# Kernel optimization log

Measured on AMD Instinct MI355X. Metric: run time of the kernel, lower is better.

The kernel has to match this reference:

```python
import jax, jax.numpy as jnp
import numpy as np

NUM_HEADS = 8
NUM_POINTS = 4


def _bilinear_sample(value_hw, locs, H, W):
    """grid_sample(mode='bilinear', align_corners=False, padding_mode='zeros').
    value_hw: [B, heads, H*W, hd]; locs: [B, Nq, heads, P, 2] in [0,1].
    Returns [B, Nq, heads, P, hd]."""
    B, Nq, heads, P, _ = locs.shape
    hd = value_hw.shape[-1]
    # torch maps g in [-1,1] -> pixel ((g+1)*size-1)/2; with g = 2*loc-1 this is loc*size - 0.5
    x = locs[..., 0] * W - 0.5
    y = locs[..., 1] * H - 0.5
    x0 = jnp.floor(x); y0 = jnp.floor(y)
    wx = x - x0; wy = y - y0
    ix0 = x0.astype(jnp.int32); iy0 = y0.astype(jnp.int32)
    ix1 = ix0 + 1; iy1 = iy0 + 1

    def gather(iy, ix):
        valid = (ix >= 0) & (ix < W) & (iy >= 0) & (iy < H)
        flat = jnp.clip(iy, 0, H - 1) * W + jnp.clip(ix, 0, W - 1)  # [B,Nq,heads,P]
        flat_t = flat.transpose(0, 2, 1, 3).reshape(B, heads, Nq * P)
        v = jnp.take_along_axis(value_hw, flat_t[..., None], axis=2)  # [B,heads,Nq*P,hd]
        v = v.reshape(B, heads, Nq, P, hd).transpose(0, 2, 1, 3, 4)
        return v * valid[..., None].astype(v.dtype)

    out = (gather(iy0, ix0) * ((1 - wx) * (1 - wy))[..., None]
           + gather(iy0, ix1) * (wx * (1 - wy))[..., None]
           + gather(iy1, ix0) * ((1 - wx) * wy)[..., None]
           + gather(iy1, ix1) * (wx * wy)[..., None])
    return out


def setup_inputs() -> dict:
    key = jax.random.key(0)
    ks = jax.random.split(key, 12)
    B, Nq, C, H, W = 4, 8192, 256, 128, 128
    heads, P = NUM_HEADS, NUM_POINTS
    s = 1.0 / np.sqrt(C)
    return {
        "query": jax.random.normal(ks[0], (B, Nq, C), jnp.float32),
        "reference_points": jax.random.uniform(ks[1], (B, Nq, 2), jnp.float32),
        "value": jax.random.normal(ks[2], (B, H * W, C), jnp.float32),
        "W_off": jax.random.normal(ks[3], (C, heads * P * 2), jnp.float32) * s,
        "b_off": jax.random.normal(ks[4], (heads * P * 2,), jnp.float32) * 0.5,
        "W_attn": jax.random.normal(ks[5], (C, heads * P), jnp.float32) * s,
        "b_attn": jax.random.normal(ks[6], (heads * P,), jnp.float32) * 0.1,
        "W_v": jax.random.normal(ks[7], (C, C), jnp.float32) * s,
        "b_v": jax.random.normal(ks[8], (C,), jnp.float32) * 0.1,
        "W_out": jax.random.normal(ks[9], (C, C), jnp.float32) * s,
        "b_out": jax.random.normal(ks[10], (C,), jnp.float32) * 0.1,
        "H": H,
        "W": W,
    }


def reference(query, reference_points, value, W_off, b_off, W_attn, b_attn,
              W_v, b_v, W_out, b_out, H, W):
    B, Nq, C = query.shape
    heads, P = NUM_HEADS, NUM_POINTS
    hd = C // heads

    offsets = (query @ W_off + b_off).reshape(B, Nq, heads, P, 2)
    attn = jax.nn.softmax((query @ W_attn + b_attn).reshape(B, Nq, heads, P), axis=-1)

    off_x = offsets[..., 0] / float(W) * 0.1
    off_y = offsets[..., 1] / float(H) * 0.1
    locs = reference_points[:, :, None, None, :] + jnp.stack([off_x, off_y], axis=-1)
    locs = jnp.clip(locs, 0.0, 1.0)  # [B,Nq,heads,P,2]

    # value projection -> [B, heads, H*W, hd]
    v = (value @ W_v + b_v).reshape(B, H * W, heads, hd).transpose(0, 2, 1, 3)

    sampled = _bilinear_sample(v, locs, H, W)            # [B,Nq,heads,P,hd]
    agg = jnp.einsum('bnhp,bnhpd->bnhd', attn, sampled)  # weighted sum over points
    out = agg.reshape(B, Nq, C) @ W_out + b_out
    return out
```

## Files before the change

kernel.cpp:

```cpp
#include <hip/hip_runtime.h>
#include <cstdint>

#define NB 4
#define NQ 8192
#define NC 256
#define IH 128
#define IW 128
#define NHW (IH * IW)
#define NHEADS 8
#define NP 4
#define NHD 32

typedef __bf16 bf16x8 __attribute__((ext_vector_type(8)));
typedef float f32x4 __attribute__((ext_vector_type(4)));

union FragCast { uint4 q; bf16x8 v; };

__device__ __forceinline__ unsigned int f2bf(float f) {
    unsigned int u = __float_as_uint(f);
    return (u + 0x7FFFu + ((u >> 16) & 1u)) >> 16;
}
__device__ __forceinline__ float bf2f(unsigned short s) {
    return __uint_as_float(((unsigned int)s) << 16);
}

__global__ __launch_bounds__(256) void k_pack(
    const float* __restrict__ Wv, const float* __restrict__ Wout,
    const float* __restrict__ Woff, const float* __restrict__ Wattn,
    unsigned short* __restrict__ pkv, unsigned short* __restrict__ pko,
    unsigned short* __restrict__ pkq)
{
    const int tid = blockIdx.x * 256 + threadIdx.x;
    if (tid < 4096) {
        const float* src = (tid & 2048) ? Wout : Wv;
        unsigned short* dst = (tid & 2048) ? pko : pkv;
        const int rem = tid & 2047;
        const int kt = rem >> 8, col = rem & 255;
        unsigned short* d = dst + (size_t)(kt * 256 + col) * 32;
        const float* s = src + (size_t)kt * 32 * 256 + col;
#pragma unroll
        for (int j = 0; j < 32; ++j)
            d[j] = (unsigned short)f2bf(s[(size_t)j * 256]);
    } else {
        const int rem = tid - 4096;
        const int kt = rem / 96, col = rem % 96;
        unsigned short* d = pkq + (size_t)(kt * 96 + col) * 32;
        const float* s; int stride;
        if (col < 64) { s = Woff + col; stride = 64; }
        else          { s = Wattn + (col - 64); stride = 32; }
        s += (size_t)kt * 32 * stride;
#pragma unroll
        for (int j = 0; j < 32; ++j)
            d[j] = (unsigned short)f2bf(s[(size_t)j * stride]);
    }
}

#define VP_TPB 4
__global__ __launch_bounds__(512) void k_vproj(
    const float* __restrict__ value, const unsigned short* __restrict__ Bpk,
    const float* __restrict__ bv, unsigned short* __restrict__ vproj)
{
    const int t = threadIdx.x;
    const int l = t & 63, w = t >> 6;
    const int mh = w & 1, cg = w >> 1;

    __shared__ unsigned short A[2][64 * 256];

    uint4 bq[8][4];
#pragma unroll
    for (int kt = 0; kt < 8; ++kt)
#pragma unroll
        for (int i = 0; i < 4; ++i)
            bq[kt][i] = *reinterpret_cast<const uint4*>(
                Bpk + (size_t)kt * 8192 + (size_t)(cg * 4 + i) * 512 +
                (l & 15) * 32 + (l >> 4) * 8);

    float bb[4];
#pragma unroll
    for (int i = 0; i < 4; ++i) bb[i] = bv[cg * 64 + i * 16 + (l & 15)];

    const size_t tile0 = (size_t)blockIdx.x * VP_TPB;

    float4 st[8];
#pragma unroll
    for (int i = 0; i < 8; ++i) {
        const int chunk = i * 512 + t;
        const int row = chunk >> 6, k0 = (chunk & 63) * 4;
        st[i] = *reinterpret_cast<const float4*>(&value[(tile0 * 64 + row) * NC + k0]);
    }
#pragma unroll
    for (int i = 0; i < 8; ++i) {
        const int chunk = i * 512 + t;
        const int row = chunk >> 6, k0 = (chunk & 63) * 4;
        unsigned int byte = (unsigned int)(row * 512 + k0 * 2) ^ (unsigned int)((row & 7) << 4);
        *reinterpret_cast<uint2*>(reinterpret_cast<char*>(A[0]) + byte) =
            make_uint2(f2bf(st[i].x) | (f2bf(st[i].y) << 16),
                       f2bf(st[i].z) | (f2bf(st[i].w) << 16));
    }
    __syncthreads();

    for (int tt = 0; tt < VP_TPB; ++tt) {
        const int cur = tt & 1;
        if (tt + 1 < VP_TPB) {
#pragma unroll
            for (int i = 0; i < 8; ++i) {
                const int chunk = i * 512 + t;
                const int row = chunk >> 6, k0 = (chunk & 63) * 4;
                st[i] = *reinterpret_cast<const float4*>(
                    &value[((tile0 + tt + 1) * 64 + row) * NC + k0]);
            }
        }

        f32x4 acc[2][4];
#pragma unroll
        for (int m = 0; m < 2; ++m)
#pragma unroll
            for (int i = 0; i < 4; ++i) acc[m][i] = (f32x4)(bb[i]);

#pragma unroll
        for (int kt = 0; kt < 8; ++kt) {
#pragma unroll
            for (int m = 0; m < 2; ++m) {
                const int arow = mh * 32 + m * 16 + (l & 15);
                unsigned int abyte = (unsigned int)(arow * 512 + (kt * 32 + (l >> 4) * 8) * 2)
                                   ^ (unsigned int)((arow & 7) << 4);
                FragCast af;
                af.q = *reinterpret_cast<const uint4*>(reinterpret_cast<const char*>(A[cur]) + abyte);
#pragma unroll
                for (int i = 0; i < 4; ++i) {
                    FragCast bfc; bfc.q = bq[kt][i];
                    acc[m][i] = __builtin_amdgcn_mfma_f32_16x16x32_bf16(af.v, bfc.v, acc[m][i], 0, 0, 0);
                }
            }
        }

        const size_t rowbase = (tile0 + tt) * 64;
#pragma unroll
        for (int m = 0; m < 2; ++m)
#pragma unroll
            for (int i = 0; i < 4; ++i) {
                const int col = cg * 64 + i * 16 + (l & 15);
#pragma unroll
                for (int j = 0; j < 4; ++j) {
                    const size_t row = rowbase + mh * 32 + m * 16 + (l >> 4) * 4 + j;
                    vproj[row * NC + col] = (unsigned short)f2bf(acc[m][i][j]);
                }
            }

        if (tt + 1 < VP_TPB) {
#pragma unroll
            for (int i = 0; i < 8; ++i) {
                const int chunk = i * 512 + t;
                const int row = chunk >> 6, k0 = (chunk & 63) * 4;
                unsigned int byte = (unsigned int)(row * 512 + k0 * 2) ^ (unsigned int)((row & 7) << 4);
                *reinterpret_cast<uint2*>(reinterpret_cast<char*>(A[cur ^ 1]) + byte) =
                    make_uint2(f2bf(st[i].x) | (f2bf(st[i].y) << 16),
                               f2bf(st[i].z) | (f2bf(st[i].w) << 16));
            }
            __syncthreads();
        }
    }
}

__global__ __launch_bounds__(256) void k_offattn(
    const float* __restrict__ query, const float* __restrict__ refp,
    const unsigned short* __restrict__ Bpk, const float* __restrict__ boff,
    const float* __restrict__ battn,
    float* __restrict__ locs, float* __restrict__ attnw)
{
    const int t = threadIdx.x;
    const int l = t & 63, w = t >> 6;
    const size_t q0 = (size_t)blockIdx.x * 32;

    __shared__ unsigned short A[32 * 256];
    __shared__ float refs[32][2];

#pragma unroll
    for (int i = 0; i < 8; ++i) {
        const int chunk = i * 256 + t;
        const int row = chunk >> 6;
        const int k0 = (chunk & 63) * 4;
        const float4 v4 = *reinterpret_cast<const float4*>(&query[(q0 + row) * NC + k0]);
        const unsigned int lo = f2bf(v4.x) | (f2bf(v4.y) << 16);
        const unsigned int hi = f2bf(v4.z) | (f2bf(v4.w) << 16);
        unsigned int byte = (unsigned int)(row * 512 + k0 * 2);
        byte ^= (unsigned int)((row & 7) << 4);
        *reinterpret_cast<uint2*>(reinterpret_cast<char*>(A) + byte) = make_uint2(lo, hi);
    }
    if (t < 64) reinterpret_cast<float*>(refs)[t] = refp[q0 * 2 + t];
    __syncthreads();

    const int rt = w >> 1, ctbase = (w & 1) * 3;
    const int arow = rt * 16 + (l & 15);
    const int achunk = l >> 4;

    f32x4 acc[3];
#pragma unroll
    for (int i = 0; i < 3; ++i) acc[i] = (f32x4)(0.f);

#pragma unroll
    for (int kt = 0; kt < 8; ++kt) {
        unsigned int abyte = (unsigned int)(arow * 512 + (kt * 32 + achunk * 8) * 2);
        abyte ^= (unsigned int)((arow & 7) << 4);
        FragCast af;
        af.q = *reinterpret_cast<const uint4*>(reinterpret_cast<const char*>(A) + abyte);
        const unsigned short* bbase = Bpk + (size_t)kt * (96 * 32) + (l & 15) * 32 + achunk * 8;
#pragma unroll
        for (int i = 0; i < 3; ++i) {
            const int ct = ctbase + i;
            FragCast bfc;
            bfc.q = *reinterpret_cast<const uint4*>(bbase + ct * 512);
            acc[i] = __builtin_amdgcn_mfma_f32_16x16x32_bf16(af.v, bfc.v, acc[i], 0, 0, 0);
        }
    }

#pragma unroll
    for (int i = 0; i < 3; ++i) {
        const int col = (ctbase + i) * 16 + (l & 15);
        if (col < 64) {
            const float bias = boff[col];
            const int xy = col & 1;
#pragma unroll
            for (int j = 0; j < 4; ++j) {
                const int row = rt * 16 + (l >> 4) * 4 + j;
                float off = acc[i][j] + bias;
                float loc = refs[row][xy] + off * (0.1f / 128.0f);
                loc = fminf(fmaxf(loc, 0.f), 1.f);
                locs[(q0 + row) * 64 + col] = loc;
            }
        } else {
            const int lc = col - 64;
            const float bias = battn[lc];
#pragma unroll
            for (int j = 0; j < 4; ++j) {
                const int row = rt * 16 + (l >> 4) * 4 + j;
                float v = acc[i][j] + bias;
                float m = fmaxf(v, __shfl_xor(v, 1));
                m = fmaxf(m, __shfl_xor(m, 2));
                float e = __expf(v - m);
                float s = e + __shfl_xor(e, 1);
                s = s + __shfl_xor(s, 2);
                attnw[(q0 + row) * 32 + lc] = e / s;
            }
        }
    }
}

__global__ __launch_bounds__(256) void k_sample(
    const unsigned short* __restrict__ vproj, const float* __restrict__ locs,
    const float* __restrict__ attnw, const unsigned short* __restrict__ Bpk,
    const float* __restrict__ bout, float* __restrict__ out)
{
    const int t = threadIdx.x;
    const int l = t & 63, w = t >> 6;
    const size_t q0 = (size_t)blockIdx.x * 16;
    const int b = (int)(q0 / NQ);

    __shared__ float locs_s[16][64];
    __shared__ float attn_s[16][32];
    __shared__ unsigned short agg[16 * 256];

    {
        const float4* ls = reinterpret_cast<const float4*>(locs + q0 * 64);
        float4* ld = reinterpret_cast<float4*>(&locs_s[0][0]);
        ld[t] = ls[t];
        const float2* as = reinterpret_cast<const float2*>(attnw + q0 * 32);
        float2* ad = reinterpret_cast<float2*>(&attn_s[0][0]);
        ad[t] = as[t];
    }
    __syncthreads();

    const int rhalf = l >> 5, h = (l >> 2) & 7, c = l & 3;
    const unsigned short* __restrict__ vb =
        vproj + (size_t)b * NHW * NC + h * NHD + c * 8;

#pragma unroll
    for (int it = 0; it < 2; ++it) {
        const int r = w * 4 + it * 2 + rhalf;
        float wts[16];
        uint4 vals[16];
#pragma unroll
        for (int p = 0; p < 4; ++p) {
            const float lx = locs_s[r][h * 8 + p * 2 + 0];
            const float ly = locs_s[r][h * 8 + p * 2 + 1];
            const float aw = attn_s[r][h * 4 + p];
            const float x = lx * (float)IW - 0.5f;
            const float y = ly * (float)IH - 0.5f;
            const float x0f = floorf(x), y0f = floorf(y);
            const float wx = x - x0f, wy = y - y0f;
            const int ix0 = (int)x0f, iy0 = (int)y0f;
            const int ix1 = ix0 + 1, iy1 = iy0 + 1;
            const int cx0 = max(ix0, 0), cy0 = max(iy0, 0);
            const int cx1 = min(ix1, IW - 1), cy1 = min(iy1, IH - 1);
            const float vx0 = (ix0 >= 0) ? 1.f : 0.f;
            const float vy0 = (iy0 >= 0) ? 1.f : 0.f;
            const float vx1 = (ix1 < IW) ? 1.f : 0.f;
            const float vy1 = (iy1 < IH) ? 1.f : 0.f;
            wts[p * 4 + 0] = aw * ((1.f - wx) * (1.f - wy) * vx0 * vy0);
            wts[p * 4 + 1] = aw * (wx * (1.f - wy) * vx1 * vy0);
            wts[p * 4 + 2] = aw * ((1.f - wx) * wy * vx0 * vy1);
            wts[p * 4 + 3] = aw * (wx * wy * vx1 * vy1);
            vals[p * 4 + 0] = *reinterpret_cast<const uint4*>(vb + (size_t)(cy0 * IW + cx0) * NC);
            vals[p * 4 + 1] = *reinterpret_cast<const uint4*>(vb + (size_t)(cy0 * IW + cx1) * NC);
            vals[p * 4 + 2] = *reinterpret_cast<const uint4*>(vb + (size_t)(cy1 * IW + cx0) * NC);
            vals[p * 4 + 3] = *reinterpret_cast<const uint4*>(vb + (size_t)(cy1 * IW + cx1) * NC);
        }
        float acc[8];
#pragma unroll
        for (int e = 0; e < 8; ++e) acc[e] = 0.f;
#pragma unroll
        for (int j = 0; j < 16; ++j) {
            const unsigned short* u = reinterpret_cast<const unsigned short*>(&vals[j]);
            const float wj = wts[j];
#pragma unroll
            for (int e = 0; e < 8; ++e) acc[e] = fmaf(wj, bf2f(u[e]), acc[e]);
        }
        uint4 pk;
        pk.x = f2bf(acc[0]) | (f2bf(acc[1]) << 16);
        pk.y = f2bf(acc[2]) | (f2bf(acc[3]) << 16);
        pk.z = f2bf(acc[4]) | (f2bf(acc[5]) << 16);
        pk.w = f2bf(acc[6]) | (f2bf(acc[7]) << 16);
        unsigned int byte = (unsigned int)(r * 512 + (h * NHD + c * 8) * 2);
        byte ^= (unsigned int)((r & 7) << 4);
        *reinterpret_cast<uint4*>(reinterpret_cast<char*>(agg) + byte) = pk;
    }
    __syncthreads();

    const int arow = l & 15;
    const int achunk = l >> 4;
    f32x4 acc2[4];
#pragma unroll
    for (int i = 0; i < 4; ++i) acc2[i] = (f32x4)(0.f);

#pragma unroll
    for (int kt = 0; kt < 8; ++kt) {
        unsigned int abyte = (unsigned int)(arow * 512 + (kt * 32 + achunk * 8) * 2);
        abyte ^= (unsigned int)((arow & 7) << 4);
        FragCast af;
        af.q = *reinterpret_cast<const uint4*>(reinterpret_cast<const char*>(agg) + abyte);
        const unsigned short* bbase = Bpk + (size_t)kt * 8192 + (l & 15) * 32 + achunk * 8;
#pragma unroll
        for (int i = 0; i < 4; ++i) {
            const int ct = w * 4 + i;
            FragCast bfc;
            bfc.q = *reinterpret_cast<const uint4*>(bbase + ct * 512);
            acc2[i] = __builtin_amdgcn_mfma_f32_16x16x32_bf16(af.v, bfc.v, acc2[i], 0, 0, 0);
        }
    }

#pragma unroll
    for (int i = 0; i < 4; ++i) {
        const int col = (w * 4 + i) * 16 + (l & 15);
        const float bbv = bout[col];
#pragma unroll
        for (int j = 0; j < 4; ++j) {
            const size_t row = q0 + (l >> 4) * 4 + j;
            out[row * NC + col] = acc2[i][j] + bbv;
        }
    }
}

extern "C" void kernel_launch(void* const* d_in, const int* in_sizes, int n_in,
                              void* d_out, int out_size, void* d_ws, size_t ws_size,
                              hipStream_t stream) {
    const float* query = (const float*)d_in[0];
    const float* refp  = (const float*)d_in[1];
    const float* value = (const float*)d_in[2];
    const float* Woff  = (const float*)d_in[3];
    const float* boff  = (const float*)d_in[4];
    const float* Wattn = (const float*)d_in[5];
    const float* battn = (const float*)d_in[6];
    const float* Wv    = (const float*)d_in[7];
    const float* bv    = (const float*)d_in[8];
    const float* Wout  = (const float*)d_in[9];
    const float* bout  = (const float*)d_in[10];
    float* out = (float*)d_out;

    unsigned short* vproj = (unsigned short*)d_ws;
    float* locs  = (float*)(vproj + (size_t)NB * NHW * NC);
    float* attnw = locs + (size_t)NB * NQ * NHEADS * NP * 2;
    unsigned short* WvPk   = (unsigned short*)(attnw + (size_t)NB * NQ * NHEADS * NP);
    unsigned short* WoutPk = WvPk + (size_t)NC * NC;
    unsigned short* WqPk   = WoutPk + (size_t)NC * NC;

    k_pack<<<dim3(19), dim3(256), 0, stream>>>(Wv, Wout, Woff, Wattn, WvPk, WoutPk, WqPk);
    k_vproj<<<dim3(256), dim3(512), 0, stream>>>(value, WvPk, bv, vproj);
    k_offattn<<<dim3(NB * NQ / 32), dim3(256), 0, stream>>>(query, refp, WqPk, boff,
                                                            battn, locs, attnw);
    k_sample<<<dim3(NB * NQ / 16), dim3(256), 0, stream>>>(vproj, locs, attnw, WoutPk, bout, out);
}
```

Before: 82.72 us.

## Fuse offset/attention projection into sampling kernel, eliminating locs/attn round-trip

Merges the query offset/attention-weight GEMM with softmax into the sampling+output-projection kernel, so locations and attention weights go straight to shared memory and never through global workspace. This removes one kernel launch and the global write/read of the locs and attnw buffers. The query tile buffer is reused for the aggregated samples, and a scheduling barrier is placed after the gather loads. In exchange, each 16-query block now does the small GEMM with uneven wave work (two of the four waves run a second pass), and the stages within a block are serialized.

```diff
diff --git a/kernel.cpp b/kernel.cpp
--- a/kernel.cpp
+++ b/kernel.cpp
@@ -162,200 +162,174 @@
     }
 }
 
-__global__ __launch_bounds__(256) void k_offattn(
+__global__ __launch_bounds__(256) void k_fused(
     const float* __restrict__ query, const float* __restrict__ refp,
-    const unsigned short* __restrict__ Bpk, const float* __restrict__ boff,
-    const float* __restrict__ battn,
-    float* __restrict__ locs, float* __restrict__ attnw)
-{
-    const int t = threadIdx.x;
-    const int l = t & 63, w = t >> 6;
-    const size_t q0 = (size_t)blockIdx.x * 32;
-
-    __shared__ unsigned short A[32 * 256];
-    __shared__ float refs[32][2];
-
-#pragma unroll
-    for (int i = 0; i < 8; ++i) {
-        const int chunk = i * 256 + t;
-        const int row = chunk >> 6;
-        const int k0 = (chunk & 63) * 4;
-        const float4 v4 = *reinterpret_cast<const float4*>(&query[(q0 + row) * NC + k0]);
-        const unsigned int lo = f2bf(v4.x) | (f2bf(v4.y) << 16);
-        const unsigned int hi = f2bf(v4.z) | (f2bf(v4.w) << 16);
-        unsigned int byte = (unsigned int)(row * 512 + k0 * 2);
-        byte ^= (unsigned int)((row & 7) << 4);
-        *reinterpret_cast<uint2*>(reinterpret_cast<char*>(A) + byte) = make_uint2(lo, hi);
-    }
-    if (t < 64) reinterpret_cast<float*>(refs)[t] = refp[q0 * 2 + t];
-    __syncthreads();
-
-    const int rt = w >> 1, ctbase = (w & 1) * 3;
-    const int arow = rt * 16 + (l & 15);
-    const int achunk = l >> 4;
-
-    f32x4 acc[3];
-#pragma unroll
-    for (int i = 0; i < 3; ++i) acc[i] = (f32x4)(0.f);
-
-#pragma unroll
-    for (int kt = 0; kt < 8; ++kt) {
-        unsigned int abyte = (unsigned int)(arow * 512 + (kt * 32 + achunk * 8) * 2);
-        abyte ^= (unsigned int)((arow & 7) << 4);
-        FragCast af;
-        af.q = *reinterpret_cast<const uint4*>(reinterpret_cast<const char*>(A) + abyte);
-        const unsigned short* bbase = Bpk + (size_t)kt * (96 * 32) + (l & 15) * 32 + achunk * 8;
-#pragma unroll
-        for (int i = 0; i < 3; ++i) {
-            const int ct = ctbase + i;
-            FragCast bfc;
-            bfc.q = *reinterpret_cast<const uint4*>(bbase + ct * 512);
-            acc[i] = __builtin_amdgcn_mfma_f32_16x16x32_bf16(af.v, bfc.v, acc[i], 0, 0, 0);
-        }
-    }
-
-#pragma unroll
-    for (int i = 0; i < 3; ++i) {
-        const int col = (ctbase + i) * 16 + (l & 15);
-        if (col < 64) {
-            const float bias = boff[col];
-            const int xy = col & 1;
-#pragma unroll
-            for (int j = 0; j < 4; ++j) {
-                const int row = rt * 16 + (l >> 4) * 4 + j;
-                float off = acc[i][j] + bias;
-                float loc = refs[row][xy] + off * (0.1f / 128.0f);
-                loc = fminf(fmaxf(loc, 0.f), 1.f);
-                locs[(q0 + row) * 64 + col] = loc;
-            }
-        } else {
-            const int lc = col - 64;
-            const float bias = battn[lc];
-#pragma unroll
-            for (int j = 0; j < 4; ++j) {
-                const int row = rt * 16 + (l >> 4) * 4 + j;
-                float v = acc[i][j] + bias;
-                float m = fmaxf(v, __shfl_xor(v, 1));
-                m = fmaxf(m, __shfl_xor(m, 2));
-                float e = __expf(v - m);
-                float s = e + __shfl_xor(e, 1);
-                s = s + __shfl_xor(s, 2);
-                attnw[(q0 + row) * 32 + lc] = e / s;
-            }
-        }
-    }
-}
-
-__global__ __launch_bounds__(256) void k_sample(
-    const unsigned short* __restrict__ vproj, const float* __restrict__ locs,
-    const float* __restrict__ attnw, const unsigned short* __restrict__ Bpk,
-    const float* __restrict__ bout, float* __restrict__ out)
+    const unsigned short* __restrict__ Bq, const float* __restrict__ boff,
+    const float* __restrict__ battn, const unsigned short* __restrict__ vproj,
+    const unsigned short* __restrict__ Bo, const float* __restrict__ bout,
+    float* __restrict__ out)
 {
     const int t = threadIdx.x;
     const int l = t & 63, w = t >> 6;
     const size_t q0 = (size_t)blockIdx.x * 16;
     const int b = (int)(q0 / NQ);
 
+    __shared__ unsigned short A[16 * 256];
     __shared__ float locs_s[16][64];
     __shared__ float attn_s[16][32];
-    __shared__ unsigned short agg[16 * 256];
+    __shared__ float refs[16][2];
+
+#pragma unroll
+    for (int i = 0; i < 4; ++i) {
+        const int chunk = i * 256 + t;
+        const int row = chunk >> 6, k0 = (chunk & 63) * 4;
+        const float4 v4 = *reinterpret_cast<const float4*>(&query[(q0 + row) * NC + k0]);
+        unsigned int byte = (unsigned int)(row * 512 + k0 * 2) ^ (unsigned int)((row & 7) << 4);
+        *reinterpret_cast<uint2*>(reinterpret_cast<char*>(A) + byte) =
+            make_uint2(f2bf(v4.x) | (f2bf(v4.y) << 16),
+                       f2bf(v4.z) | (f2bf(v4.w) << 16));
+    }
+    if (t < 32) reinterpret_cast<float*>(refs)[t] = refp[q0 * 2 + t];
+    __syncthreads();
 
     {
-        const float4* ls = reinterpret_cast<const float4*>(locs + q0 * 64);
-        float4* ld = reinterpret_cast<float4*>(&locs_s[0][0]);
-        ld[t] = ls[t];
-        const float2* as = reinterpret_cast<const float2*>(attnw + q0 * 32);
-        float2* ad = reinterpret_cast<float2*>(&attn_s[0][0]);
-        ad[t] = as[t];
+        const int arow = l & 15, achunk = l >> 4;
+#pragma unroll
+        for (int pass = 0; pass < 2; ++pass) {
+            if (pass == 1 && w >= 2) break;
+            const int ct = pass == 0 ? w : 4 + w;
+            f32x4 acc = (f32x4)(0.f);
+#pragma unroll
+            for (int kt = 0; kt < 8; ++kt) {
+                unsigned int abyte = (unsigned int)(arow * 512 + (kt * 32 + achunk * 8) * 2)
+                                   ^ (unsigned int)((arow & 7) << 4);
+                FragCast af;
+                af.q = *reinterpret_cast<const uint4*>(reinterpret_cast<const char*>(A) + abyte);
+                FragCast bfc;
+                bfc.q = *reinterpret_cast<const uint4*>(
+                    Bq + (size_t)kt * 3072 + (size_t)(ct * 16 + arow) * 32 + achunk * 8);
+                acc = __builtin_amdgcn_mfma_f32_16x16x32_bf16(af.v, bfc.v, acc, 0, 0, 0);
+            }
+            const int col = ct * 16 + arow;
+            if (col < 64) {
+                const float bias = boff[col];
+                const int xy = col & 1;
+#pragma unroll
+                for (int j = 0; j < 4; ++j) {
+                    const int row = achunk * 4 + j;
+                    float off = acc[j] + bias;
+                    float loc = refs[row][xy] + off * (0.1f / 128.0f);
+                    locs_s[row][col] = fminf(fmaxf(loc, 0.f), 1.f);
+                }
+            } else {
+                const int lc = col - 64;
+                const float bias = battn[lc];
+#pragma unroll
+                for (int j = 0; j < 4; ++j) {
+                    const int row = achunk * 4 + j;
+                    float v = acc[j] + bias;
+                    float m = fmaxf(v, __shfl_xor(v, 1));
+                    m = fmaxf(m, __shfl_xor(m, 2));
+                    float e = __expf(v - m);
+                    float s = e + __shfl_xor(e, 1);
+                    s = s + __shfl_xor(s, 2);
+                    attn_s[row][lc] = e / s;
+                }
+            }
+        }
     }
     __syncthreads();
 
-    const int rhalf = l >> 5, h = (l >> 2) & 7, c = l & 3;
-    const unsigned short* __restrict__ vb =
-        vproj + (size_t)b * NHW * NC + h * NHD + c * 8;
-
-#pragma unroll
-    for (int it = 0; it < 2; ++it) {
-        const int r = w * 4 + it * 2 + rhalf;
-        float wts[16];
-        uint4 vals[16];
-#pragma unroll
-        for (int p = 0; p < 4; ++p) {
-            const float lx = locs_s[r][h * 8 + p * 2 + 0];
-            const float ly = locs_s[r][h * 8 + p * 2 + 1];
-            const float aw = attn_s[r][h * 4 + p];
-            const float x = lx * (float)IW - 0.5f;
-            const float y = ly * (float)IH - 0.5f;
-            const float x0f = floorf(x), y0f = floorf(y);
-            const float wx = x - x0f, wy = y - y0f;
-            const int ix0 = (int)x0f, iy0 = (int)y0f;
-            const int ix1 = ix0 + 1, iy1 = iy0 + 1;
-            const int cx0 = max(ix0, 0), cy0 = max(iy0, 0);
-            const int cx1 = min(ix1, IW - 1), cy1 = min(iy1, IH - 1);
-            const float vx0 = (ix0 >= 0) ? 1.f : 0.f;
-            const float vy0 = (iy0 >= 0) ? 1.f : 0.f;
-            const float vx1 = (ix1 < IW) ? 1.f : 0.f;
-            const float vy1 = (iy1 < IH) ? 1.f : 0.f;
-            wts[p * 4 + 0] = aw * ((1.f - wx) * (1.f - wy) * vx0 * vy0);
-            wts[p * 4 + 1] = aw * (wx * (1.f - wy) * vx1 * vy0);
-            wts[p * 4 + 2] = aw * ((1.f - wx) * wy * vx0 * vy1);
-            wts[p * 4 + 3] = aw * (wx * wy * vx1 * vy1);
-            vals[p * 4 + 0] = *reinterpret_cast<const uint4*>(vb + (size_t)(cy0 * IW + cx0) * NC);
-            vals[p * 4 + 1] = *reinterpret_cast<const uint4*>(vb + (size_t)(cy0 * IW + cx1) * NC);
-            vals[p * 4 + 2] = *reinterpret_cast<const uint4*>(vb + (size_t)(cy1 * IW + cx0) * NC);
-            vals[p * 4 + 3] = *reinterpret_cast<const uint4*>(vb + (size_t)(cy1 * IW + cx1) * NC);
-        }
-        float acc[8];
-#pragma unroll
-        for (int e = 0; e < 8; ++e) acc[e] = 0.f;
-#pragma unroll
-        for (int j = 0; j < 16; ++j) {
-            const unsigned short* u = reinterpret_cast<const unsigned short*>(&vals[j]);
-            const float wj = wts[j];
-#pragma unroll
-            for (int e = 0; e < 8; ++e) acc[e] = fmaf(wj, bf2f(u[e]), acc[e]);
-        }
-        uint4 pk;
-        pk.x = f2bf(acc[0]) | (f2bf(acc[1]) << 16);
-        pk.y = f2bf(acc[2]) | (f2bf(acc[3]) << 16);
-        pk.z = f2bf(acc[4]) | (f2bf(acc[5]) << 16);
-        pk.w = f2bf(acc[6]) | (f2bf(acc[7]) << 16);
-        unsigned int byte = (unsigned int)(r * 512 + (h * NHD + c * 8) * 2);
-        byte ^= (unsigned int)((r & 7) << 4);
-        *reinterpret_cast<uint4*>(reinterpret_cast<char*>(agg) + byte) = pk;
+    {
+        const int rhalf = l >> 5, h = (l >> 2) & 7, c = l & 3;
+        const unsigned short* __restrict__ vb =
+            vproj + (size_t)b * NHW * NC + h * NHD + c * 8;
+
+#pragma unroll
+        for (int it = 0; it < 2; ++it) {
+            const int r = w * 4 + it * 2 + rhalf;
+            float wts[16];
+            uint4 vals[16];
+#pragma unroll
+            for (int p = 0; p < 4; ++p) {
+                const float lx = locs_s[r][h * 8 + p * 2 + 0];
+                const float ly = locs_s[r][h * 8 + p * 2 + 1];
+                const float aw = attn_s[r][h * 4 + p];
+                const float x = lx * (float)IW - 0.5f;
+                const float y = ly * (float)IH - 0.5f;
+                const float x0f = floorf(x), y0f = floorf(y);
+                const float wx = x - x0f, wy = y - y0f;
+                const int ix0 = (int)x0f, iy0 = (int)y0f;
+                const int ix1 = ix0 + 1, iy1 = iy0 + 1;
+                const int cx0 = max(ix0, 0), cy0 = max(iy0, 0);
+                const int cx1 = min(ix1, IW - 1), cy1 = min(iy1, IH - 1);
+                const float vx0 = (ix0 >= 0) ? 1.f : 0.f;
+                const float vy0 = (iy0 >= 0) ? 1.f : 0.f;
+                const float vx1 = (ix1 < IW) ? 1.f : 0.f;
+                const float vy1 = (iy1 < IH) ? 1.f : 0.f;
+                wts[p * 4 + 0] = aw * ((1.f - wx) * (1.f - wy) * vx0 * vy0);
+                wts[p * 4 + 1] = aw * (wx * (1.f - wy) * vx1 * vy0);
+                wts[p * 4 + 2] = aw * ((1.f - wx) * wy * vx0 * vy1);
+                wts[p * 4 + 3] = aw * (wx * wy * vx1 * vy1);
+                vals[p * 4 + 0] = *reinterpret_cast<const uint4*>(vb + (size_t)(cy0 * IW + cx0) * NC);
+                vals[p * 4 + 1] = *reinterpret_cast<const uint4*>(vb + (size_t)(cy0 * IW + cx1) * NC);
+                vals[p * 4 + 2] = *reinterpret_cast<const uint4*>(vb + (size_t)(cy1 * IW + cx0) * NC);
+                vals[p * 4 + 3] = *reinterpret_cast<const uint4*>(vb + (size_t)(cy1 * IW + cx1) * NC);
+            }
+            __builtin_amdgcn_sched_barrier(0);
+            float acc[8];
+#pragma unroll
+            for (int e = 0; e < 8; ++e) acc[e] = 0.f;
+#pragma unroll
+            for (int j = 0; j < 16; ++j) {
+                const unsigned short* u = reinterpret_cast<const unsigned short*>(&vals[j]);
+                const float wj = wts[j];
+#pragma unroll
+                for (int e = 0; e < 8; ++e) acc[e] = fmaf(wj, bf2f(u[e]), acc[e]);
+            }
+            uint4 pk;
+            pk.x = f2bf(acc[0]) | (f2bf(acc[1]) << 16);
+            pk.y = f2bf(acc[2]) | (f2bf(acc[3]) << 16);
+            pk.z = f2bf(acc[4]) | (f2bf(acc[5]) << 16);
+            pk.w = f2bf(acc[6]) | (f2bf(acc[7]) << 16);
+            unsigned int byte = (unsigned int)(r * 512 + (h * NHD + c * 8) * 2)
+                              ^ (unsigned int)((r & 7) << 4);
+            *reinterpret_cast<uint4*>(reinterpret_cast<char*>(A) + byte) = pk;
+        }
     }
     __syncthreads();
 
-    const int arow = l & 15;
-    const int achunk = l >> 4;
-    f32x4 acc2[4];
-#pragma unroll
-    for (int i = 0; i < 4; ++i) acc2[i] = (f32x4)(0.f);
-
-#pragma unroll
-    for (int kt = 0; kt < 8; ++kt) {
-        unsigned int abyte = (unsigned int)(arow * 512 + (kt * 32 + achunk * 8) * 2);
-        abyte ^= (unsigned int)((arow & 7) << 4);
-        FragCast af;
-        af.q = *reinterpret_cast<const uint4*>(reinterpret_cast<const char*>(agg) + abyte);
-        const unsigned short* bbase = Bpk + (size_t)kt * 8192 + (l & 15) * 32 + achunk * 8;
+    {
+        const int arow = l & 15, achunk = l >> 4;
+        f32x4 acc2[4];
+#pragma unroll
+        for (int i = 0; i < 4; ++i) acc2[i] = (f32x4)(0.f);
+
+#pragma unroll
+        for (int kt = 0; kt < 8; ++kt) {
+            unsigned int abyte = (unsigned int)(arow * 512 + (kt * 32 + achunk * 8) * 2)
+                               ^ (unsigned int)((arow & 7) << 4);
+            FragCast af;
+            af.q = *reinterpret_cast<const uint4*>(reinterpret_cast<const char*>(A) + abyte);
+            const unsigned short* bbase = Bo + (size_t)kt * 8192 + arow * 32 + achunk * 8;
+#pragma unroll
+            for (int i = 0; i < 4; ++i) {
+                const int ct = w * 4 + i;
+                FragCast bfc;
+                bfc.q = *reinterpret_cast<const uint4*>(bbase + (size_t)ct * 512);
+                acc2[i] = __builtin_amdgcn_mfma_f32_16x16x32_bf16(af.v, bfc.v, acc2[i], 0, 0, 0);
+            }
+        }
+
 #pragma unroll
         for (int i = 0; i < 4; ++i) {
-            const int ct = w * 4 + i;
-            FragCast bfc;
-            bfc.q = *reinterpret_cast<const uint4*>(bbase + ct * 512);
-            acc2[i] = __builtin_amdgcn_mfma_f32_16x16x32_bf16(af.v, bfc.v, acc2[i], 0, 0, 0);
-        }
-    }
-
-#pragma unroll
-    for (int i = 0; i < 4; ++i) {
-        const int col = (w * 4 + i) * 16 + (l & 15);
-        const float bbv = bout[col];
-#pragma unroll
-        for (int j = 0; j < 4; ++j) {
-            const size_t row = q0 + (l >> 4) * 4 + j;
-            out[row * NC + col] = acc2[i][j] + bbv;
+            const int col = (w * 4 + i) * 16 + arow;
+            const float bbv = bout[col];
+#pragma unroll
+            for (int j = 0; j < 4; ++j) {
+                const size_t row = q0 + achunk * 4 + j;
+                out[row * NC + col] = acc2[i][j] + bbv;
+            }
         }
     }
 }
@@ -376,16 +350,13 @@
     const float* bout  = (const float*)d_in[10];
     float* out = (float*)d_out;
 
-    unsigned short* vproj = (unsigned short*)d_ws;
-    float* locs  = (float*)(vproj + (size_t)NB * NHW * NC);
-    float* attnw = locs + (size_t)NB * NQ * NHEADS * NP * 2;
-    unsigned short* WvPk   = (unsigned short*)(attnw + (size_t)NB * NQ * NHEADS * NP);
+    unsigned short* vproj  = (unsigned short*)d_ws;
+    unsigned short* WvPk   = vproj + (size_t)NB * NHW * NC;
     unsigned short* WoutPk = WvPk + (size_t)NC * NC;
     unsigned short* WqPk   = WoutPk + (size_t)NC * NC;
 
     k_pack<<<dim3(19), dim3(256), 0, stream>>>(Wv, Wout, Woff, Wattn, WvPk, WoutPk, WqPk);
     k_vproj<<<dim3(256), dim3(512), 0, stream>>>(value, WvPk, bv, vproj);
-    k_offattn<<<dim3(NB * NQ / 32), dim3(256), 0, stream>>>(query, refp, WqPk, boff,
-                                                            battn, locs, attnw);
-    k_sample<<<dim3(NB * NQ / 16), dim3(256), 0, stream>>>(vproj, locs, attnw, WoutPk, bout, out);
-}
+    k_fused<<<dim3(NB * NQ / 16), dim3(256), 0, stream>>>(query, refp, WqPk, boff, battn,
+                                                          vproj, WoutPk, bout, out);
+}
```

Measured after the change: 74.13 us. 1.12x faster.

## Store value projection per batch-head plane and split sampling from output projection

Applied to the files above, without the earlier changes.

The value projection is now written as contiguous [B, head, pixel, 32] planes instead of [B, pixel, 256]. The fused sample+outproj kernel is split into a gather kernel, where each block handles one (batch, head) pair for 64 queries, and a separate double-buffered MFMA output-projection kernel that keeps weights in registers. The goal is better cache locality for the gathers, since each head plane is 1 MB, and more efficient GEMM tiling. The cost is an extra round trip for the bf16 aggregate through global memory, one more launch, and scattered 2-byte stores in vproj.

```diff
diff --git a/kernel.cpp b/kernel.cpp
--- a/kernel.cpp
+++ b/kernel.cpp
@@ -140,10 +140,13 @@
 #pragma unroll
             for (int i = 0; i < 4; ++i) {
                 const int col = cg * 64 + i * 16 + (l & 15);
+                const int hh = col >> 5, dd = col & 31;
 #pragma unroll
                 for (int j = 0; j < 4; ++j) {
                     const size_t row = rowbase + mh * 32 + m * 16 + (l >> 4) * 4 + j;
-                    vproj[row * NC + col] = (unsigned short)f2bf(acc[m][i][j]);
+                    const size_t bidx = row >> 14, pix = row & (NHW - 1);
+                    vproj[(((bidx << 3) + hh) * (size_t)NHW + pix) * NHD + dd] =
+                        (unsigned short)f2bf(acc[m][i][j]);
                 }
             }
 
@@ -246,116 +249,193 @@
     }
 }
 
-__global__ __launch_bounds__(256) void k_sample(
+__global__ __launch_bounds__(256) void k_gather(
     const unsigned short* __restrict__ vproj, const float* __restrict__ locs,
-    const float* __restrict__ attnw, const unsigned short* __restrict__ Bpk,
+    const float* __restrict__ attnw, unsigned short* __restrict__ agg)
+{
+    const int bid = blockIdx.x;
+    const int x = bid & 7;
+    const int rem = bid >> 3;
+    const int pg = rem >> 7;
+    const int chunk = rem & 127;
+    const int pair = pg * 8 + x;
+    const int b = pair >> 3, h = pair & 7;
+    const int t = threadIdx.x;
+
+    const size_t qrow0 = (size_t)b * NQ + chunk * 64;
+
+    __shared__ float lc[64][8];
+    __shared__ float at[64][4];
+
+    if (t < 128) {
+        const int q = t >> 1, part = t & 1;
+        *reinterpret_cast<float4*>(&lc[q][part * 4]) =
+            *reinterpret_cast<const float4*>(&locs[(qrow0 + q) * 64 + h * 8 + part * 4]);
+    } else if (t < 192) {
+        const int q = t - 128;
+        *reinterpret_cast<float4*>(&at[q][0]) =
+            *reinterpret_cast<const float4*>(&attnw[(qrow0 + q) * 32 + h * 4]);
+    }
+    __syncthreads();
+
+    const int q = t >> 2, c = t & 3;
+    const char* __restrict__ plane =
+        reinterpret_cast<const char*>(vproj + (size_t)pair * NHW * NHD);
+    const unsigned int laneoff = (unsigned int)(c * 16);
+
+    float wts[16];
+    unsigned int offs[16];
+#pragma unroll
+    for (int p = 0; p < 4; ++p) {
+        const float lx = lc[q][p * 2 + 0];
+        const float ly = lc[q][p * 2 + 1];
+        const float aw = at[q][p];
+        const float xx = lx * (float)IW - 0.5f;
+        const float yy = ly * (float)IH - 0.5f;
+        const float x0f = floorf(xx), y0f = floorf(yy);
+        const float wx = xx - x0f, wy = yy - y0f;
+        const int ix0 = (int)x0f, iy0 = (int)y0f;
+        const int ix1 = ix0 + 1, iy1 = iy0 + 1;
+        const int cx0 = max(ix0, 0), cy0 = max(iy0, 0);
+        const int cx1 = min(ix1, IW - 1), cy1 = min(iy1, IH - 1);
+        const float vx0 = (ix0 >= 0) ? 1.f : 0.f;
+        const float vy0 = (iy0 >= 0) ? 1.f : 0.f;
+        const float vx1 = (ix1 < IW) ? 1.f : 0.f;
+        const float vy1 = (iy1 < IH) ? 1.f : 0.f;
+        wts[p * 4 + 0] = aw * ((1.f - wx) * (1.f - wy) * vx0 * vy0);
+        wts[p * 4 + 1] = aw * (wx * (1.f - wy) * vx1 * vy0);
+        wts[p * 4 + 2] = aw * ((1.f - wx) * wy * vx0 * vy1);
+        wts[p * 4 + 3] = aw * (wx * wy * vx1 * vy1);
+        offs[p * 4 + 0] = (unsigned int)(cy0 * IW + cx0) * 64u + laneoff;
+        offs[p * 4 + 1] = (unsigned int)(cy0 * IW + cx1) * 64u + laneoff;
+        offs[p * 4 + 2] = (unsigned int)(cy1 * IW + cx0) * 64u + laneoff;
+        offs[p * 4 + 3] = (unsigned int)(cy1 * IW + cx1) * 64u + laneoff;
+    }
+
+    uint4 vals[16];
+#pragma unroll
+    for (int j = 0; j < 16; ++j)
+        vals[j] = *reinterpret_cast<const uint4*>(plane + offs[j]);
+
+    float acc[8];
+#pragma unroll
+    for (int e = 0; e < 8; ++e) acc[e] = 0.f;
+#pragma unroll
+    for (int j = 0; j < 16; ++j) {
+        const unsigned short* u = reinterpret_cast<const unsigned short*>(&vals[j]);
+        const float wj = wts[j];
+#pragma unroll
+        for (int e = 0; e < 8; ++e) acc[e] = fmaf(wj, bf2f(u[e]), acc[e]);
+    }
+
+    uint4 pk;
+    pk.x = f2bf(acc[0]) | (f2bf(acc[1]) << 16);
+    pk.y = f2bf(acc[2]) | (f2bf(acc[3]) << 16);
+    pk.z = f2bf(acc[4]) | (f2bf(acc[5]) << 16);
+    pk.w = f2bf(acc[6]) | (f2bf(acc[7]) << 16);
+    *reinterpret_cast<uint4*>(&agg[(qrow0 + q) * NC + h * NHD + c * 8]) = pk;
+}
+
+#define OP_TPB 4
+__global__ __launch_bounds__(512) void k_outproj(
+    const unsigned short* __restrict__ agg, const unsigned short* __restrict__ Bpk,
     const float* __restrict__ bout, float* __restrict__ out)
 {
     const int t = threadIdx.x;
     const int l = t & 63, w = t >> 6;
-    const size_t q0 = (size_t)blockIdx.x * 16;
-    const int b = (int)(q0 / NQ);
-
-    __shared__ float locs_s[16][64];
-    __shared__ float attn_s[16][32];
-    __shared__ unsigned short agg[16 * 256];
-
-    {
-        const float4* ls = reinterpret_cast<const float4*>(locs + q0 * 64);
-        float4* ld = reinterpret_cast<float4*>(&locs_s[0][0]);
-        ld[t] = ls[t];
-        const float2* as = reinterpret_cast<const float2*>(attnw + q0 * 32);
-        float2* ad = reinterpret_cast<float2*>(&attn_s[0][0]);
-        ad[t] = as[t];
+    const int mh = w & 1, cg = w >> 1;
+
+    __shared__ unsigned short A[2][64 * 256];
+
+    uint4 bq[8][4];
+#pragma unroll
+    for (int kt = 0; kt < 8; ++kt)
+#pragma unroll
+        for (int i = 0; i < 4; ++i)
+            bq[kt][i] = *reinterpret_cast<const uint4*>(
+                Bpk + (size_t)kt * 8192 + (size_t)(cg * 4 + i) * 512 +
+                (l & 15) * 32 + (l >> 4) * 8);
+
+    float bb[4];
+#pragma unroll
+    for (int i = 0; i < 4; ++i) bb[i] = bout[cg * 64 + i * 16 + (l & 15)];
+
+    const size_t tile0 = (size_t)blockIdx.x * OP_TPB;
+
+    uint4 st[4];
+#pragma unroll
+    for (int i = 0; i < 4; ++i) {
+        const int chunk = i * 512 + t;
+        const int row = chunk >> 5, o16 = (chunk & 31) * 16;
+        st[i] = *reinterpret_cast<const uint4*>(
+            reinterpret_cast<const char*>(agg) + (tile0 * 64 + row) * 512 + o16);
+    }
+#pragma unroll
+    for (int i = 0; i < 4; ++i) {
+        const int chunk = i * 512 + t;
+        const int row = chunk >> 5, o16 = (chunk & 31) * 16;
+        unsigned int byte = (unsigned int)(row * 512 + o16) ^ (unsigned int)((row & 7) << 4);
+        *reinterpret_cast<uint4*>(reinterpret_cast<char*>(A[0]) + byte) = st[i];
     }
     __syncthreads();
 
-    const int rhalf = l >> 5, h = (l >> 2) & 7, c = l & 3;
-    const unsigned short* __restrict__ vb =
-        vproj + (size_t)b * NHW * NC + h * NHD + c * 8;
-
-#pragma unroll
-    for (int it = 0; it < 2; ++it) {
-        const int r = w * 4 + it * 2 + rhalf;
-        float wts[16];
-        uint4 vals[16];
-#pragma unroll
-        for (int p = 0; p < 4; ++p) {
-            const float lx = locs_s[r][h * 8 + p * 2 + 0];
-            const float ly = locs_s[r][h * 8 + p * 2 + 1];
-            const float aw = attn_s[r][h * 4 + p];
-            const float x = lx * (float)IW - 0.5f;
-            const float y = ly * (float)IH - 0.5f;
-            const float x0f = floorf(x), y0f = floorf(y);
-            const float wx = x - x0f, wy = y - y0f;
-            const int ix0 = (int)x0f, iy0 = (int)y0f;
-            const int ix1 = ix0 + 1, iy1 = iy0 + 1;
-            const int cx0 = max(ix0, 0), cy0 = max(iy0, 0);
-            const int cx1 = min(ix1, IW - 1), cy1 = min(iy1, IH - 1);
-            const float vx0 = (ix0 >= 0) ? 1.f : 0.f;
-            const float vy0 = (iy0 >= 0) ? 1.f : 0.f;
-            const float vx1 = (ix1 < IW) ? 1.f : 0.f;
-            const float vy1 = (iy1 < IH) ? 1.f : 0.f;
-            wts[p * 4 + 0] = aw * ((1.f - wx) * (1.f - wy) * vx0 * vy0);
-            wts[p * 4 + 1] = aw * (wx * (1.f - wy) * vx1 * vy0);
-            wts[p * 4 + 2] = aw * ((1.f - wx) * wy * vx0 * vy1);
-            wts[p * 4 + 3] = aw * (wx * wy * vx1 * vy1);
-            vals[p * 4 + 0] = *reinterpret_cast<const uint4*>(vb + (size_t)(cy0 * IW + cx0) * NC);
-            vals[p * 4 + 1] = *reinterpret_cast<const uint4*>(vb + (size_t)(cy0 * IW + cx1) * NC);
-            vals[p * 4 + 2] = *reinterpret_cast<const uint4*>(vb + (size_t)(cy1 * IW + cx0) * NC);
-            vals[p * 4 + 3] = *reinterpret_cast<const uint4*>(vb + (size_t)(cy1 * IW + cx1) * NC);
-        }
-        float acc[8];
-#pragma unroll
-        for (int e = 0; e < 8; ++e) acc[e] = 0.f;
-#pragma unroll
-        for (int j = 0; j < 16; ++j) {
-            const unsigned short* u = reinterpret_cast<const unsigned short*>(&vals[j]);
-            const float wj = wts[j];
-#pragma unroll
-            for (int e = 0; e < 8; ++e) acc[e] = fmaf(wj, bf2f(u[e]), acc[e]);
-        }
-        uint4 pk;
-        pk.x = f2bf(acc[0]) | (f2bf(acc[1]) << 16);
-        pk.y = f2bf(acc[2]) | (f2bf(acc[3]) << 16);
-        pk.z = f2bf(acc[4]) | (f2bf(acc[5]) << 16);
-        pk.w = f2bf(acc[6]) | (f2bf(acc[7]) << 16);
-        unsigned int byte = (unsigned int)(r * 512 + (h * NHD + c * 8) * 2);
-        byte ^= (unsigned int)((r & 7) << 4);
-        *reinterpret_cast<uint4*>(reinterpret_cast<char*>(agg) + byte) = pk;
-    }
-    __syncthreads();
-
-    const int arow = l & 15;
-    const int achunk = l >> 4;
-    f32x4 acc2[4];
-#pragma unroll
-    for (int i = 0; i < 4; ++i) acc2[i] = (f32x4)(0.f);
-
-#pragma unroll
-    for (int kt = 0; kt < 8; ++kt) {
-        unsigned int abyte = (unsigned int)(arow * 512 + (kt * 32 + achunk * 8) * 2);
-        abyte ^= (unsigned int)((arow & 7) << 4);
-        FragCast af;
-        af.q = *reinterpret_cast<const uint4*>(reinterpret_cast<const char*>(agg) + abyte);
-        const unsigned short* bbase = Bpk + (size_t)kt * 8192 + (l & 15) * 32 + achunk * 8;
-#pragma unroll
-        for (int i = 0; i < 4; ++i) {
-            const int ct = w * 4 + i;
-            FragCast bfc;
-            bfc.q = *reinterpret_cast<const uint4*>(bbase + ct * 512);
-            acc2[i] = __builtin_amdgcn_mfma_f32_16x16x32_bf16(af.v, bfc.v, acc2[i], 0, 0, 0);
-        }
-    }
-
-#pragma unroll
-    for (int i = 0; i < 4; ++i) {
-        const int col = (w * 4 + i) * 16 + (l & 15);
-        const float bbv = bout[col];
-#pragma unroll
-        for (int j = 0; j < 4; ++j) {
-            const size_t row = q0 + (l >> 4) * 4 + j;
-            out[row * NC + col] = acc2[i][j] + bbv;
+    for (int tt = 0; tt < OP_TPB; ++tt) {
+        const int cur = tt & 1;
+        if (tt + 1 < OP_TPB) {
+#pragma unroll
+            for (int i = 0; i < 4; ++i) {
+                const int chunk = i * 512 + t;
+                const int row = chunk >> 5, o16 = (chunk & 31) * 16;
+                st[i] = *reinterpret_cast<const uint4*>(
+                    reinterpret_cast<const char*>(agg) + ((tile0 + tt + 1) * 64 + row) * 512 + o16);
+            }
+        }
+
+        f32x4 acc[2][4];
+#pragma unroll
+        for (int m = 0; m < 2; ++m)
+#pragma unroll
+            for (int i = 0; i < 4; ++i) acc[m][i] = (f32x4)(bb[i]);
+
+#pragma unroll
+        for (int kt = 0; kt < 8; ++kt) {
+#pragma unroll
+            for (int m = 0; m < 2; ++m) {
+                const int arow = mh * 32 + m * 16 + (l & 15);
+                unsigned int abyte = (unsigned int)(arow * 512 + (kt * 32 + (l >> 4) * 8) * 2)
+                                   ^ (unsigned int)((arow & 7) << 4);
+                FragCast af;
+                af.q = *reinterpret_cast<const uint4*>(reinterpret_cast<const char*>(A[cur]) + abyte);
+#pragma unroll
+                for (int i = 0; i < 4; ++i) {
+                    FragCast bfc; bfc.q = bq[kt][i];
+                    acc[m][i] = __builtin_amdgcn_mfma_f32_16x16x32_bf16(af.v, bfc.v, acc[m][i], 0, 0, 0);
+                }
+            }
+        }
+
+        const size_t rowbase = (tile0 + tt) * 64;
+#pragma unroll
+        for (int m = 0; m < 2; ++m)
+#pragma unroll
+            for (int i = 0; i < 4; ++i) {
+                const int col = cg * 64 + i * 16 + (l & 15);
+#pragma unroll
+                for (int j = 0; j < 4; ++j) {
+                    const size_t row = rowbase + mh * 32 + m * 16 + (l >> 4) * 4 + j;
+                    out[row * NC + col] = acc[m][i][j];
+                }
+            }
+
+        if (tt + 1 < OP_TPB) {
+#pragma unroll
+            for (int i = 0; i < 4; ++i) {
+                const int chunk = i * 512 + t;
+                const int row = chunk >> 5, o16 = (chunk & 31) * 16;
+                unsigned int byte = (unsigned int)(row * 512 + o16) ^ (unsigned int)((row & 7) << 4);
+                *reinterpret_cast<uint4*>(reinterpret_cast<char*>(A[cur ^ 1]) + byte) = st[i];
+            }
+            __syncthreads();
         }
     }
 }
@@ -376,10 +456,11 @@
     const float* bout  = (const float*)d_in[10];
     float* out = (float*)d_out;
 
-    unsigned short* vproj = (unsigned short*)d_ws;
+    unsigned short* vproj  = (unsigned short*)d_ws;
     float* locs  = (float*)(vproj + (size_t)NB * NHW * NC);
     float* attnw = locs + (size_t)NB * NQ * NHEADS * NP * 2;
-    unsigned short* WvPk   = (unsigned short*)(attnw + (size_t)NB * NQ * NHEADS * NP);
+    unsigned short* agg   = (unsigned short*)(attnw + (size_t)NB * NQ * NHEADS * NP);
+    unsigned short* WvPk   = agg + (size_t)NB * NQ * NC;
     unsigned short* WoutPk = WvPk + (size_t)NC * NC;
     unsigned short* WqPk   = WoutPk + (size_t)NC * NC;
 
@@ -387,5 +468,6 @@
     k_vproj<<<dim3(256), dim3(512), 0, stream>>>(value, WvPk, bv, vproj);
     k_offattn<<<dim3(NB * NQ / 32), dim3(256), 0, stream>>>(query, refp, WqPk, boff,
                                                             battn, locs, attnw);
-    k_sample<<<dim3(NB * NQ / 16), dim3(256), 0, stream>>>(vproj, locs, attnw, WoutPk, bout, out);
-}
+    k_gather<<<dim3(NB * NHEADS * (NQ / 64)), dim3(256), 0, stream>>>(vproj, locs, attnw, agg);
+    k_outproj<<<dim3(NB * NQ / (64 * OP_TPB)), dim3(512), 0, stream>>>(agg, WoutPk, bout, out);
+}
```

After: 88.47 us. +7.0%, slower.
